# Optimization experiments

Hardware: AMD Instinct MI355X
Metric: run time of the kernel (lower is better)

The kernel has to match this reference:

```python
import jax, jax.numpy as jnp
import numpy as np

D = 1024      # embedding_dim
FW = 64       # filter_width
DEPTH = 2     # recurrence_depth
E = D * (DEPTH + 1)  # expanded dim = 3072
B, L = 2, 4096


def setup_inputs() -> dict:
    key = jax.random.key(0)
    ks = jax.random.split(key, 12)
    s = lambda k, shape, scale: jax.random.normal(k, shape, dtype=jnp.float32) * scale
    return {
        "x": jax.random.normal(ks[0], (B, L, D), dtype=jnp.float32),
        # input_projection: Linear(D, E)  (stored as [in,out])
        "w_in": s(ks[1], (D, E), 0.02), "b_in": jnp.zeros((E,), jnp.float32),
        # depthwise Conv1d(E, E, k=3, padding=2, groups=E): torch weight [E,1,3]
        "w_conv": s(ks[2], (E, 1, 3), 0.5), "b_conv": jnp.zeros((E,), jnp.float32),
        # HyenaFilter MLP: Linear(3,FW) -> SiLU -> Linear(FW,FW) -> SiLU -> Linear(FW, D, bias=False)
        "w1": s(ks[3], (3, FW), 0.5), "b1": jnp.zeros((FW,), jnp.float32),
        "w2": s(ks[4], (FW, FW), 0.1), "b2": jnp.zeros((FW,), jnp.float32),
        "w3": s(ks[5], (FW, D), 0.1),
        # HyenaFilter.bias parameter (output_channels = D*(DEPTH-1) = D)
        "filt_bias": jax.random.normal(ks[6], (D,), dtype=jnp.float32),
        # output_projection: Linear(D, D)
        "w_out": s(ks[7], (D, D), 0.02), "b_out": jnp.zeros((D,), jnp.float32),
    }


def _fftconv(x_bdl, h, bias_d):
    Lq = x_bdl.shape[-1]
    n = 2 * Lq
    Xf = jnp.fft.rfft(x_bdl, n=n)                       # [b,d,n//2+1]
    Hf = jnp.fft.rfft(h, n=n) / n                       # broadcast over [b,d]
    y = jnp.fft.irfft(Xf * Hf, n=n, norm="forward")[..., :Lq]
    return y + x_bdl * bias_d[:, None]


def reference(x, w_in, b_in, w_conv, b_conv, w1, b1, w2, b2, w3, filt_bias, w_out, b_out):
    _, Lx, Dm = x.shape
    # expand_input: Linear then b l e -> b e l
    u = (x @ w_in + b_in).transpose(0, 2, 1)            # [B,E,L]
    # depthwise short conv, padding=2 then truncate to L (causal-ish, as in source)
    u = jax.lax.conv_general_dilated(
        u, w_conv, window_strides=(1,), padding=[(2, 2)],
        feature_group_count=u.shape[1], dimension_numbers=("NCH", "OIH", "NCH"))
    u = (u + b_conv[None, :, None])[..., :Lx]
    streams = [u[:, i * Dm:(i + 1) * Dm, :] for i in range(DEPTH + 1)]  # each [B,D,L]
    # implicit filter generation
    t = jnp.linspace(0.0, 1.0, Lx)                       # [L]
    pos = jnp.tile(t[:, None], (1, 3))                   # [L,3]
    hmlp = jax.nn.silu(pos @ w1 + b1)
    hmlp = jax.nn.silu(hmlp @ w2 + b2)
    filters = (hmlp @ w3) * jnp.exp(-t[:, None] * jnp.abs(filt_bias)[None, :])  # [L,D]
    # recurrence (depth=2 -> single gated long conv); source indexes filters by ROW i
    v = streams[-1]
    for i in range(DEPTH - 1):
        v = v * streams[i]
        v = _fftconv(v, filters[i], filt_bias)
    # merge with stream 0, back to [B,L,D], output projection
    out = (v * streams[0]).transpose(0, 2, 1) @ w_out + b_out
    return out
```

## Files before the change

### kernel.cpp

```cpp
#include <hip/hip_runtime.h>
#include <hip/hip_bf16.h>


typedef __bf16 bf16x8 __attribute__((ext_vector_type(8)));
typedef float  f32x4  __attribute__((ext_vector_type(4)));

typedef const __attribute__((address_space(1))) unsigned int GU32;
typedef __attribute__((address_space(3))) unsigned int LU32;
#define GLL16(gp, lp) __builtin_amdgcn_global_load_lds((GU32*)(gp), (LU32*)(lp), 16, 0, 0)

__device__ __forceinline__ float silu(float x) { return x / (1.f + __expf(-x)); }

__global__ __launch_bounds__(256) void hgen(const float* __restrict__ b1,
                                            const float* __restrict__ w2,
                                            const float* __restrict__ b2,
                                            const float* __restrict__ w3,
                                            float* __restrict__ h) {
    __shared__ float hm2[64];
    int t = threadIdx.x;
    if (t < 64) {
        float acc = b2[t];
        for (int f = 0; f < 64; ++f) acc += silu(b1[f]) * w2[f * 64 + t];
        hm2[t] = silu(acc);
    }
    __syncthreads();
    for (int r = 0; r < 4; ++r) {
        int j = t * 4 + r;
        float acc = 0.f;
        for (int g = 0; g < 64; ++g) acc += hm2[g] * w3[g * 1024 + j];
        h[j] = acc;
    }
}

__global__ void hfrag(const float* __restrict__ h, __bf16* __restrict__ af) {
    int sp = blockIdx.x;
    int lane = threadIdx.x;
    int m = lane & 15, kh = lane >> 4;
    bf16x8 v;
    #pragma unroll
    for (int j = 0; j < 8; ++j) {
        int k = kh * 8 + j;
        int idx = (k < 16) ? (32 * sp + m - k) : (32 * sp + 32 + m - k);
        float val = (idx >= 0 && idx < 1024) ? h[idx] : 0.f;
        v[j] = (__bf16)val;
    }
    *(bf16x8*)&af[(size_t)(sp * 64 + lane) * 8] = v;
}

__global__ __launch_bounds__(256) void cvt_x(const float* __restrict__ x,
                                             __bf16* __restrict__ xb) {
    size_t i = ((size_t)blockIdx.x * 256 + threadIdx.x) * 8;
    f32x4 a = *(const f32x4*)&x[i];
    f32x4 b = *(const f32x4*)&x[i + 4];
    bf16x8 v;
    v[0] = (__bf16)a[0]; v[1] = (__bf16)a[1]; v[2] = (__bf16)a[2]; v[3] = (__bf16)a[3];
    v[4] = (__bf16)b[0]; v[5] = (__bf16)b[1]; v[6] = (__bf16)b[2]; v[7] = (__bf16)b[3];
    *(bf16x8*)&xb[i] = v;
}

__global__ __launch_bounds__(256) void tcvt(const float* __restrict__ src,
                                            __bf16* __restrict__ dst,
                                            int ld, int cbase) {
    __shared__ __bf16 tile[64][65];
    int t = threadIdx.x;
    int k0 = blockIdx.x * 64, n0 = blockIdx.y * 64;
    int c = t & 63, rg = t >> 6;
    #pragma unroll
    for (int i = 0; i < 16; ++i) {
        int r = rg * 16 + i;
        tile[r][c] = (__bf16)src[(size_t)(k0 + r) * ld + cbase + n0 + c];
    }
    __syncthreads();
    #pragma unroll
    for (int i = 0; i < 16; ++i) {
        int nn = rg * 16 + i;
        dst[(size_t)(n0 + nn) * 1024 + k0 + c] = tile[c][nn];
    }
}

template<int EPI>
__global__ __launch_bounds__(256) void gemm128(const __bf16* __restrict__ A,
                                               const __bf16* __restrict__ Bt,
                                               const float* __restrict__ bias,
                                               void* __restrict__ out0,
                                               void* __restrict__ out1) {
    __shared__ __bf16 As[128 * 32];
    __shared__ __bf16 Bs[128 * 32];
    int t = threadIdx.x, lane = t & 63, w = t >> 6;
    int m0 = blockIdx.x * 128, n0 = blockIdx.y * 128;
    int wr = (w >> 1) * 64, wc = (w & 1) * 64;
    f32x4 acc[4][4] = {};

    int s1 = w * 64 + lane;
    int s2 = s1 + 256;
    const __bf16* a1 = A + (size_t)(m0 + (s1 >> 2)) * 1024 + (s1 & 3) * 8;
    const __bf16* a2 = A + (size_t)(m0 + (s2 >> 2)) * 1024 + (s2 & 3) * 8;
    const __bf16* b1 = Bt + (size_t)(n0 + (s1 >> 2)) * 1024 + (s1 & 3) * 8;
    const __bf16* b2 = Bt + (size_t)(n0 + (s2 >> 2)) * 1024 + (s2 & 3) * 8;

    for (int kk = 0; kk < 1024; kk += 32) {
        GLL16(a1 + kk, &As[(size_t)s1 * 8]);
        GLL16(a2 + kk, &As[(size_t)s2 * 8]);
        GLL16(b1 + kk, &Bs[(size_t)s1 * 8]);
        GLL16(b2 + kk, &Bs[(size_t)s2 * 8]);
        __syncthreads();
        int kh = (lane >> 4) * 8, rl = lane & 15;
        bf16x8 af[4], bf[4];
        #pragma unroll
        for (int i = 0; i < 4; ++i) {
            af[i] = *(const bf16x8*)&As[(wr + i * 16 + rl) * 32 + kh];
            bf[i] = *(const bf16x8*)&Bs[(wc + i * 16 + rl) * 32 + kh];
        }
        #pragma unroll
        for (int mi = 0; mi < 4; ++mi)
            #pragma unroll
            for (int ni = 0; ni < 4; ++ni)
                acc[mi][ni] = __builtin_amdgcn_mfma_f32_16x16x32_bf16(af[mi], bf[ni], acc[mi][ni], 0, 0, 0);
        __syncthreads();
    }

    int cb = lane & 15, rb = (lane >> 4) * 4;
    #pragma unroll
    for (int ni = 0; ni < 4; ++ni) {
        int col = n0 + wc + ni * 16 + cb;
        if (EPI == 0) {
            __bf16* uo = (col < 1024) ? (__bf16*)out0 : (__bf16*)out1;
            int oc = col & 1023;
            float bv = bias[(col < 1024) ? col : 1024 + col];
            #pragma unroll
            for (int mi = 0; mi < 4; ++mi) {
                int row = m0 + wr + mi * 16 + rb;
                #pragma unroll
                for (int j = 0; j < 4; ++j)
                    uo[(size_t)(row + j) * 1024 + oc] = (__bf16)(acc[mi][ni][j] + bv);
            }
        } else {
            float* o = (float*)out0;
            float bv = bias[col];
            #pragma unroll
            for (int mi = 0; mi < 4; ++mi) {
                int row = m0 + wr + mi * 16 + rb;
                #pragma unroll
                for (int j = 0; j < 4; ++j)
                    o[(size_t)(row + j) * 1024 + col] = acc[mi][ni][j] + bv;
            }
        }
    }
}

__global__ __launch_bounds__(256) void convmul(const __bf16* __restrict__ u0,
                                               const __bf16* __restrict__ u2,
                                               const float* __restrict__ w_conv,
                                               const float* __restrict__ b_conv,
                                               __bf16* __restrict__ v,
                                               __bf16* __restrict__ st) {
    __shared__ float vt[64][65];
    int t = threadIdx.x;
    int b = blockIdx.z;
    int l0b = blockIdx.x * 64;
    int d0 = blockIdx.y * 64;
    int d = t & 63, lg = t >> 6;
    int col = d0 + d;
    int l0 = l0b + lg * 16;

    float c00 = w_conv[col * 3 + 0], c01 = w_conv[col * 3 + 1], c02 = w_conv[col * 3 + 2];
    float bc0 = b_conv[col];
    int e2 = 2048 + col;
    float c20 = w_conv[e2 * 3 + 0], c21 = w_conv[e2 * 3 + 1], c22 = w_conv[e2 * 3 + 2];
    float bc2 = b_conv[e2];

    size_t base = ((size_t)b * 4096 + l0) * 1024 + col;
    float p01 = (l0 >= 1) ? (float)u0[base - 1024] : 0.f;
    float p02 = (l0 >= 2) ? (float)u0[base - 2048] : 0.f;
    float p21 = (l0 >= 1) ? (float)u2[base - 1024] : 0.f;
    float p22 = (l0 >= 2) ? (float)u2[base - 2048] : 0.f;
    #pragma unroll
    for (int il = 0; il < 16; ++il) {
        float c0v = (float)u0[base + (size_t)il * 1024];
        float c2v = (float)u2[base + (size_t)il * 1024];
        float s0v = c00 * p02 + c01 * p01 + c02 * c0v + bc0;
        float s2v = c20 * p22 + c21 * p21 + c22 * c2v + bc2;
        p02 = p01; p01 = c0v; p22 = p21; p21 = c2v;
        vt[lg * 16 + il][d] = s0v * s2v;
        st[base + (size_t)il * 1024] = (__bf16)s0v;
    }
    __syncthreads();
    int lo = t & 63, dg = t >> 6;
    size_t obase = ((size_t)b * 1024 + d0 + dg * 16) * 4096 + l0b + lo;
    #pragma unroll
    for (int id = 0; id < 16; ++id)
        v[obase + (size_t)id * 4096] = (__bf16)vt[lo][dg * 16 + id];
}

__global__ __launch_bounds__(256) void firk(const __bf16* __restrict__ v,
                                            const __bf16* __restrict__ afg,
                                            const float* __restrict__ filt_bias,
                                            __bf16* __restrict__ z) {
    __shared__ __bf16 vlds[768 * 8];
    __shared__ __bf16 alds[33 * 64 * 8];
    int t = threadIdx.x;
    int bd = blockIdx.x;
    int d = bd & 1023;
    const __bf16* vrow = v + (size_t)bd * 4096;

    for (int c = t; c < 33 * 64; c += 256)
        *(bf16x8*)&alds[c * 8] = *(const bf16x8*)&afg[(size_t)c * 8];
    #pragma unroll
    for (int i = 0; i < 3; ++i) {
        int c = t + i * 256;
        bf16x8 val = {};
        if (c >= 130 && c < 642) val = *(const bf16x8*)&vrow[(c - 130) * 8];
        int cs = c ^ ((c >> 3) & 7);
        *(bf16x8*)&vlds[cs * 8] = val;
    }
    __syncthreads();

    int lane = t & 63, w = t >> 6;
    int n = lane & 15, kh = lane >> 4;
    int khoff = (kh == 0) ? 0 : (kh == 1) ? 8 : (kh == 2) ? -16 : -8;
    f32x4 acc[4] = {};
    for (int sp = 0; sp < 33; ++sp) {
        bf16x8 af = *(const bf16x8*)&alds[(sp * 64 + lane) * 8];
        #pragma unroll
        for (int ct = 0; ct < 4; ++ct) {
            int p = w * 64 + ct * 16 + n;
            int e = 16 * p - 32 * sp + 1040 + khoff;
            int c = e >> 3;
            int cs = c ^ ((c >> 3) & 7);
            bf16x8 bfv = *(const bf16x8*)&vlds[cs * 8];
            acc[ct] = __builtin_amdgcn_mfma_f32_16x16x32_bf16(af, bfv, acc[ct], 0, 0, 0);
        }
    }

    float fb = filt_bias[d];
    __bf16* zrow = z + (size_t)bd * 4096;
    #pragma unroll
    for (int ct = 0; ct < 4; ++ct) {
        int p = w * 64 + ct * 16 + n;
        #pragma unroll
        for (int j = 0; j < 4; ++j) {
            int l = 16 * p + kh * 4 + j;
            int e = l + 1040;
            int c = e >> 3;
            int cs = c ^ ((c >> 3) & 7);
            float vv = (float)vlds[cs * 8 + (e & 7)];
            zrow[l] = (__bf16)(acc[ct][j] + vv * fb);
        }
    }
}

__global__ __launch_bounds__(256) void trz(const __bf16* __restrict__ zz,
                                           const __bf16* __restrict__ st,
                                           __bf16* __restrict__ zt) {
    __shared__ __bf16 tile[64][65];
    int t = threadIdx.x;
    int l0 = blockIdx.x * 64, d0 = blockIdx.y * 64, b = blockIdx.z;
    int c = t & 63, rg = t >> 6;
    #pragma unroll
    for (int i = 0; i < 16; ++i) {
        int r = rg * 16 + i;
        tile[r][c] = zz[((size_t)(b * 1024 + d0 + r)) * 4096 + l0 + c];
    }
    __syncthreads();
    #pragma unroll
    for (int i = 0; i < 16; ++i) {
        int li = rg * 16 + i;
        size_t o = ((size_t)b * 4096 + l0 + li) * 1024 + d0 + c;
        zt[o] = (__bf16)((float)tile[c][li] * (float)st[o]);
    }
}

extern "C" void kernel_launch(void* const* d_in, const int* in_sizes, int n_in,
                              void* d_out, int out_size, void* d_ws, size_t ws_size,
                              hipStream_t stream) {
    const float* x      = (const float*)d_in[0];
    const float* w_in   = (const float*)d_in[1];
    const float* b_in   = (const float*)d_in[2];
    const float* w_conv = (const float*)d_in[3];
    const float* b_conv = (const float*)d_in[4];
    const float* b1     = (const float*)d_in[6];
    const float* w2     = (const float*)d_in[7];
    const float* b2     = (const float*)d_in[8];
    const float* w3     = (const float*)d_in[9];
    const float* fb     = (const float*)d_in[10];
    const float* w_out  = (const float*)d_in[11];
    const float* b_out  = (const float*)d_in[12];
    float* out = (float*)d_out;

    char* ws = (char*)d_ws;
    float*  h  = (float*)ws;
    __bf16* af = (__bf16*)(ws + 4096);
    const size_t SEG = (size_t)8192 * 1024;
    __bf16* X  = (__bf16*)(ws + 40960);
    __bf16* U0 = X + SEG;
    __bf16* U2 = U0 + SEG;
    __bf16* ST = U2 + SEG;
    __bf16* WT = ST + SEG - (size_t)2048 * 1024;

    hgen<<<1, 256, 0, stream>>>(b1, w2, b2, w3, h);
    hfrag<<<33, 64, 0, stream>>>(h, af);
    cvt_x<<<4096, 256, 0, stream>>>(x, X);
    tcvt<<<dim3(16, 16), 256, 0, stream>>>(w_in, WT, 3072, 0);
    tcvt<<<dim3(16, 16), 256, 0, stream>>>(w_in, WT + (size_t)1024 * 1024, 3072, 2048);
    gemm128<0><<<dim3(64, 16), 256, 0, stream>>>(X, WT, b_in, U0, U2);
    convmul<<<dim3(64, 16, 2), 256, 0, stream>>>(U0, U2, w_conv, b_conv, X, ST);
    firk<<<2048, 256, 0, stream>>>(X, af, fb, U2);
    tcvt<<<dim3(16, 16), 256, 0, stream>>>(w_out, X, 1024, 0);
    trz<<<dim3(64, 16, 2), 256, 0, stream>>>(U2, ST, U0);
    gemm128<1><<<dim3(64, 8), 256, 0, stream>>>(U0, X, b_out, (void*)out, nullptr);
}
```

Baseline: 272.7 us.

## Replace input-projection GEMM with 256x256 double-buffered pipelined MFMA kernel

Adds a new gemm256 kernel for the input projection. It uses 512 threads, 256x256 tiles, a K-step of 64 and double-buffered LDS (128KB) filled with global_load_lds. The A and B loads for the next K-tile are interleaved with MFMA phases, with sched barriers and setprio, and an XOR swizzle avoids LDS bank conflicts. The aim is to hide global-load latency and raise MFMA utilisation over the single-buffered 128x128 kernel. In exchange, occupancy drops to one block per CU and only 256 blocks are launched, which risks under-filling the GPU.

```diff
diff --git a/kernel.cpp b/kernel.cpp
--- a/kernel.cpp
+++ b/kernel.cpp
@@ -8,6 +8,11 @@
 typedef const __attribute__((address_space(1))) unsigned int GU32;
 typedef __attribute__((address_space(3))) unsigned int LU32;
 #define GLL16(gp, lp) __builtin_amdgcn_global_load_lds((GU32*)(gp), (LU32*)(lp), 16, 0, 0)
+
+#define CFENCE asm volatile("" ::: "memory")
+#define SBAR   do { CFENCE; __builtin_amdgcn_s_barrier(); CFENCE; } while (0)
+#define SCHEDB __builtin_amdgcn_sched_barrier(0)
+#define VMCNT0 asm volatile("s_waitcnt vmcnt(0)" ::: "memory")
 
 __device__ __forceinline__ float silu(float x) { return x / (1.f + __expf(-x)); }
 
@@ -75,6 +80,138 @@
     for (int i = 0; i < 16; ++i) {
         int nn = rg * 16 + i;
         dst[(size_t)(n0 + nn) * 1024 + k0 + c] = tile[c][nn];
+    }
+}
+
+__device__ __forceinline__ void stage_half(const __bf16* __restrict__ panel, int kk,
+                                           char* ldshalf, int t) {
+    int c1 = t, c2 = t + 512;
+    int s1 = c1 ^ (((c1 >> 5) & 1) << 1);
+    int s2 = c2 ^ (((c2 >> 5) & 1) << 1);
+    GLL16(panel + (size_t)(s1 >> 3) * 1024 + kk + (s1 & 7) * 8, ldshalf + c1 * 16);
+    GLL16(panel + (size_t)(s2 >> 3) * 1024 + kk + (s2 & 7) * 8, ldshalf + c2 * 16);
+}
+
+__global__ __launch_bounds__(512, 1) void gemm256(const __bf16* __restrict__ A,
+                                                  const __bf16* __restrict__ Bt,
+                                                  const float* __restrict__ bias,
+                                                  __bf16* __restrict__ out0,
+                                                  __bf16* __restrict__ out1) {
+    __shared__ __bf16 lds[65536];
+    char* L = (char*)lds;
+    int t = threadIdx.x, lane = t & 63, w = t >> 6;
+    int wr = w >> 2, wc = w & 3;
+    int m0 = blockIdx.x * 256, n0 = blockIdx.y * 256;
+    int rl = lane & 15, kh8 = (lane >> 4) * 8;
+    int nloc = (wc & 1) * 64;
+
+    const __bf16* pa0 = A + (size_t)m0 * 1024;
+    const __bf16* pa1 = A + (size_t)(m0 + 128) * 1024;
+    const __bf16* pb0 = Bt + (size_t)n0 * 1024;
+    const __bf16* pb1 = Bt + (size_t)(n0 + 128) * 1024;
+
+    f32x4 acc[8][4] = {};
+    bf16x8 ar[4][2], br[4][2];
+
+#define RDA(dst, mf, ks) do { int _a = bA + ((mf) * 16 + rl) * 128 + ((ks) * 32 + kh8) * 2; \
+        _a ^= ((_a >> 9) & 1) << 5; dst = *(const bf16x8*)(L + _a); } while (0)
+#define RDB(dst, nf, ks) do { int _a = bB + (nloc + (nf) * 16 + rl) * 128 + ((ks) * 32 + kh8) * 2; \
+        _a ^= ((_a >> 9) & 1) << 5; dst = *(const bf16x8*)(L + _a); } while (0)
+
+    stage_half(pa0, 0, L, t);
+    stage_half(pa1, 0, L + 16384, t);
+    stage_half(pb0, 0, L + 65536, t);
+    stage_half(pb1, 0, L + 65536 + 16384, t);
+    VMCNT0;
+    SBAR;
+
+    for (int kt = 0; kt < 16; ++kt) {
+        int p = kt & 1, q = p ^ 1;
+        int bA = p * 32768 + wr * 16384;
+        int bB = 65536 + p * 32768 + (wc >> 1) * 16384;
+        int kk1 = (kt + 1) * 64;
+
+        #pragma unroll
+        for (int i = 0; i < 4; ++i) { RDA(ar[i][0], i, 0); RDA(ar[i][1], i, 1); }
+        RDB(br[0][0], 0, 0); RDB(br[0][1], 0, 1);
+        RDB(br[1][0], 1, 0); RDB(br[1][1], 1, 1);
+        if (kt < 15) {
+            stage_half(pa0, kk1, L + q * 32768, t);
+            stage_half(pa1, kk1, L + q * 32768 + 16384, t);
+        }
+        SCHEDB; SBAR; SCHEDB;
+        __builtin_amdgcn_s_setprio(1);
+        #pragma unroll
+        for (int mf = 0; mf < 4; ++mf)
+            #pragma unroll
+            for (int nf = 0; nf < 2; ++nf)
+                #pragma unroll
+                for (int ks = 0; ks < 2; ++ks)
+                    acc[mf][nf] = __builtin_amdgcn_mfma_f32_16x16x32_bf16(ar[mf][ks], br[nf][ks], acc[mf][nf], 0, 0, 0);
+        __builtin_amdgcn_s_setprio(0);
+        SCHEDB; SBAR; SCHEDB;
+
+        RDB(br[2][0], 2, 0); RDB(br[2][1], 2, 1);
+        RDB(br[3][0], 3, 0); RDB(br[3][1], 3, 1);
+        if (kt < 15) {
+            stage_half(pb0, kk1, L + 65536 + q * 32768, t);
+            stage_half(pb1, kk1, L + 65536 + q * 32768 + 16384, t);
+        }
+        SCHEDB; SBAR; SCHEDB;
+        __builtin_amdgcn_s_setprio(1);
+        #pragma unroll
+        for (int mf = 0; mf < 4; ++mf)
+            #pragma unroll
+            for (int nf = 2; nf < 4; ++nf)
+                #pragma unroll
+                for (int ks = 0; ks < 2; ++ks)
+                    acc[mf][nf] = __builtin_amdgcn_mfma_f32_16x16x32_bf16(ar[mf][ks], br[nf][ks], acc[mf][nf], 0, 0, 0);
+        __builtin_amdgcn_s_setprio(0);
+        SCHEDB; SBAR; SCHEDB;
+
+        #pragma unroll
+        for (int i = 0; i < 4; ++i) { RDA(ar[i][0], 4 + i, 0); RDA(ar[i][1], 4 + i, 1); }
+        SCHEDB; SBAR; SCHEDB;
+        __builtin_amdgcn_s_setprio(1);
+        #pragma unroll
+        for (int mf = 0; mf < 4; ++mf)
+            #pragma unroll
+            for (int nf = 0; nf < 2; ++nf)
+                #pragma unroll
+                for (int ks = 0; ks < 2; ++ks)
+                    acc[4 + mf][nf] = __builtin_amdgcn_mfma_f32_16x16x32_bf16(ar[mf][ks], br[nf][ks], acc[4 + mf][nf], 0, 0, 0);
+        __builtin_amdgcn_s_setprio(0);
+        SCHEDB; SBAR; SCHEDB;
+
+        __builtin_amdgcn_s_setprio(1);
+        #pragma unroll
+        for (int mf = 0; mf < 4; ++mf)
+            #pragma unroll
+            for (int nf = 2; nf < 4; ++nf)
+                #pragma unroll
+                for (int ks = 0; ks < 2; ++ks)
+                    acc[4 + mf][nf] = __builtin_amdgcn_mfma_f32_16x16x32_bf16(ar[mf][ks], br[nf][ks], acc[4 + mf][nf], 0, 0, 0);
+        __builtin_amdgcn_s_setprio(0);
+        VMCNT0;
+        SCHEDB; SBAR; SCHEDB;
+    }
+#undef RDA
+#undef RDB
+
+    int cb = lane & 15, rb = (lane >> 4) * 4;
+    #pragma unroll
+    for (int nf = 0; nf < 4; ++nf) {
+        int col = n0 + wc * 64 + nf * 16 + cb;
+        __bf16* uo = (col < 1024) ? out0 : out1;
+        int oc = col & 1023;
+        float bv = bias[(col < 1024) ? col : 1024 + col];
+        #pragma unroll
+        for (int mf = 0; mf < 8; ++mf) {
+            int row = m0 + wr * 128 + mf * 16 + rb;
+            #pragma unroll
+            for (int j = 0; j < 4; ++j)
+                uo[(size_t)(row + j) * 1024 + oc] = (__bf16)(acc[mf][nf][j] + bv);
+        }
     }
 }
 
@@ -99,10 +236,10 @@
     const __bf16* b2 = Bt + (size_t)(n0 + (s2 >> 2)) * 1024 + (s2 & 3) * 8;
 
     for (int kk = 0; kk < 1024; kk += 32) {
-        GLL16(a1 + kk, &As[(size_t)s1 * 8]);
-        GLL16(a2 + kk, &As[(size_t)s2 * 8]);
-        GLL16(b1 + kk, &Bs[(size_t)s1 * 8]);
-        GLL16(b2 + kk, &Bs[(size_t)s2 * 8]);
+        GLL16(a1 + kk, (char*)&As[(size_t)s1 * 8]);
+        GLL16(a2 + kk, (char*)&As[(size_t)s2 * 8]);
+        GLL16(b1 + kk, (char*)&Bs[(size_t)s1 * 8]);
+        GLL16(b2 + kk, (char*)&Bs[(size_t)s2 * 8]);
         __syncthreads();
         int kh = (lane >> 4) * 8, rl = lane & 15;
         bf16x8 af[4], bf[4];
@@ -302,7 +439,7 @@
     cvt_x<<<4096, 256, 0, stream>>>(x, X);
     tcvt<<<dim3(16, 16), 256, 0, stream>>>(w_in, WT, 3072, 0);
     tcvt<<<dim3(16, 16), 256, 0, stream>>>(w_in, WT + (size_t)1024 * 1024, 3072, 2048);
-    gemm128<0><<<dim3(64, 16), 256, 0, stream>>>(X, WT, b_in, U0, U2);
+    gemm256<<<dim3(32, 8), 512, 0, stream>>>(X, WT, b_in, U0, U2);
     convmul<<<dim3(64, 16, 2), 256, 0, stream>>>(U0, U2, w_conv, b_conv, X, ST);
     firk<<<2048, 256, 0, stream>>>(X, af, fb, U2);
     tcvt<<<dim3(16, 16), 256, 0, stream>>>(w_out, X, 1024, 0);
```

Result: no change. 268.3 us (-1.6%).
